# Kernel optimization log

Measured on AMD Instinct MI355X. Metric: run time of the kernel, lower is better.

The kernel has to match this reference:

```python
import jax, jax.numpy as jnp
import numpy as np

N_WORDS = 500000
N_LABELS = 64
PAD_INDEX = 0
UNK_INDEX = 1
BATCH, SEQ_LEN = 8192, 512


def setup_inputs() -> dict:
    key = jax.random.key(0)
    kw, kl, klen = jax.random.split(key, 3)
    # sequence lengths in [S/2, S]; pads go at the end (loop semantics assume contiguous prefix)
    lens = jax.random.randint(klen, (BATCH,), SEQ_LEN // 2, SEQ_LEN + 1)
    words = jax.random.randint(kw, (BATCH, SEQ_LEN), 2, N_WORDS, dtype=jnp.int32)
    labels = jax.random.randint(kl, (BATCH, SEQ_LEN), 0, N_LABELS, dtype=jnp.int32)
    pos = jnp.arange(SEQ_LEN, dtype=jnp.int32)[None, :]
    words = jnp.where(pos < lens[:, None], words, PAD_INDEX)
    trans_count = jnp.zeros((N_LABELS + 1, N_LABELS + 1), jnp.float32)
    emit_count = jnp.zeros((N_WORDS, N_LABELS), jnp.float32)
    return {"words": words, "labels": labels,
            "trans_count": trans_count, "emit_count": emit_count}


def reference(words, labels, trans_count, emit_count):
    # Vectorized equivalent of the double Python loop of scalar increments.
    B, S = words.shape
    lens = (words != PAD_INDEX).sum(-1)                       # [B]
    valid = jnp.arange(S, dtype=lens.dtype)[None, :] < lens[:, None]  # [B,S]
    wgt = valid.astype(trans_count.dtype).ravel()             # 1.0 for counted tokens
    ext_words = jnp.where(words >= N_WORDS, UNK_INDEX, words)
    # pre label: -1 (== last index N_LABELS) at j=0, else labels[:, j-1]
    pre = jnp.concatenate(
        [jnp.full((B, 1), N_LABELS, labels.dtype), labels[:, :-1]], axis=1)
    # trans_count[t, pre] += 1  (flattened scatter-add)
    t_flat = (labels.astype(jnp.int32) * (N_LABELS + 1) + pre.astype(jnp.int32)).ravel()
    tc = trans_count.ravel().at[t_flat].add(wgt).reshape(trans_count.shape)
    # emit_count[w, t] += 1
    e_flat = (ext_words.astype(jnp.int32) * N_LABELS + labels.astype(jnp.int32)).ravel()
    ec = emit_count.ravel().at[e_flat].add(wgt).reshape(emit_count.shape)
    return tc, ec
```

## Files before the change

### kernel.cpp

```cpp
#include <hip/hip_runtime.h>
#include <hip/hip_bf16.h>


constexpr int N_WORDS  = 500000;
constexpr int N_LABELS = 64;
constexpr int SEQ_LEN  = 512;
constexpr int BINS     = (N_LABELS + 1) * (N_LABELS + 1);
constexpr int N_CELLS  = N_WORDS * N_LABELS;
constexpr int P        = 1000;
constexpr int CPP      = 32000;
constexpr int TILE_TOK = 8192;
constexpr int QPT      = TILE_TOK / 4;
constexpr int B1 = 1024, G1 = 512;
constexpr int B2 = 1024;
constexpr int MAXTILES = 1024;
constexpr int FIN_BLOCKS = 5;
constexpr size_t DYN2 = (size_t)(CPP / 2 + MAXTILES) * sizeof(unsigned);


__global__ __launch_bounds__(B1)
void phase1(const int* __restrict__ words, const int* __restrict__ labels,
            unsigned* __restrict__ dir,
            unsigned short* __restrict__ keys,
            unsigned* __restrict__ part_t,
            int n, int ntiles) {
    __shared__ unsigned trans[BINS];
    __shared__ unsigned keybuf[TILE_TOK];
    __shared__ unsigned short sorted[TILE_TOK];
    __shared__ unsigned cnt[1024];
    __shared__ unsigned wsum[16];
    const int tid  = threadIdx.x;
    const int lane = tid & 63;
    for (int k = tid; k < BINS; k += B1) trans[k] = 0u;

    const int nquads = n >> 2;
    for (int tile = blockIdx.x; tile < ntiles; tile += gridDim.x) {
        const int q0 = tile * QPT;
        const int tq = min(QPT, nquads - q0);
        cnt[tid] = 0u;
        __syncthreads();

        for (int lq = tid; lq < tq; lq += B1) {
            const int q = q0 + lq;
            const int i = q << 2;
            const int4 w4 = reinterpret_cast<const int4*>(words)[q];
            const int4 l4 = reinterpret_cast<const int4*>(labels)[q];
            const int j0 = i & (SEQ_LEN - 1);
            int pre = (j0 == 0) ? N_LABELS : labels[i - 1];
            int wv[4] = {w4.x, w4.y, w4.z, w4.w};
            int lv[4] = {l4.x, l4.y, l4.z, l4.w};
            unsigned pk[4];
            #pragma unroll
            for (int k = 0; k < 4; ++k) {
                const int lab = lv[k];
                unsigned pack = 0xFFFFFFFFu;
                if (wv[k] != 0) {
                    atomicAdd(&trans[lab * (N_LABELS + 1) + pre], 1u);
                    const int w = (wv[k] >= N_WORDS) ? 1 : wv[k];
                    const unsigned key = (unsigned)w * N_LABELS + (unsigned)lab;
                    const unsigned p   = key / CPP;
                    pack = (p << 16) | (key - p * CPP);
                    atomicAdd(&cnt[p], 1u);
                }
                pk[k] = pack;
                pre = lab;
            }
            reinterpret_cast<uint4*>(keybuf)[lq] = make_uint4(pk[0], pk[1], pk[2], pk[3]);
        }
        __syncthreads();

        {
            const unsigned c = cnt[tid];
            unsigned v = c;
            #pragma unroll
            for (int d = 1; d < 64; d <<= 1) {
                const unsigned u = __shfl_up(v, d, 64);
                if (lane >= d) v += u;
            }
            if (lane == 63) wsum[tid >> 6] = v;
            __syncthreads();
            if (tid < 16) {
                const unsigned s = wsum[tid];
                unsigned vv = s;
                #pragma unroll
                for (int d = 1; d < 16; d <<= 1) {
                    const unsigned u = __shfl_up(vv, d, 64);
                    if (tid >= d) vv += u;
                }
                wsum[tid] = vv - s;
            }
            __syncthreads();
            const unsigned off = v - c + wsum[tid >> 6];
            cnt[tid] = off;
            if (tid < P) dir[(size_t)tile * P + tid] = (c << 16) | off;
        }
        __syncthreads();

        const int tt = tq << 2;
        for (int t = tid; t < tt; t += B1) {
            const unsigned pack = keybuf[t];
            if (pack != 0xFFFFFFFFu) {
                const unsigned s = atomicAdd(&cnt[pack >> 16], 1u);
                sorted[s] = (unsigned short)(pack & 0xFFFFu);
            }
        }
        __syncthreads();

        reinterpret_cast<uint4*>(keys + (size_t)tile * TILE_TOK)[tid] =
            reinterpret_cast<const uint4*>(sorted)[tid];
        __syncthreads();
    }

    unsigned* my = part_t + (size_t)blockIdx.x * BINS;
    for (int k = tid; k < BINS; k += B1) my[k] = trans[k];
}


__global__ __launch_bounds__(B2)
void phase2(const unsigned* __restrict__ dir,
            const unsigned short* __restrict__ keys,
            const unsigned* __restrict__ part_t,
            float* __restrict__ out, int ntiles) {
    extern __shared__ unsigned h[];
    unsigned* dcol = h + CPP / 2;
    const unsigned bid = blockIdx.x;

    if (bid < (unsigned)FIN_BLOCKS) {
        const int k = bid * B2 + threadIdx.x;
        if (k < BINS) {
            unsigned s = 0;
            #pragma unroll 8
            for (int pb = 0; pb < G1; ++pb) s += part_t[(size_t)pb * BINS + k];
            out[k] = (float)s;
        }
        return;
    }
    const unsigned p = bid - FIN_BLOCKS;

    for (int t = threadIdx.x; t < ntiles; t += B2)
        dcol[t] = dir[(size_t)t * P + p];

    for (int j = threadIdx.x; j < CPP / 8; j += B2)
        reinterpret_cast<uint4*>(h)[j] = make_uint4(0u, 0u, 0u, 0u);
    __syncthreads();

    const int nseg = ntiles << 1;
    for (int s = threadIdx.x; s < nseg; s += B2) {
        const int t = s >> 1, half = s & 1;
        const unsigned e = dcol[t];
        const unsigned c = e >> 16;
        const unsigned mid = (c + 1u) >> 1;
        const unsigned i0 = half ? mid : 0u;
        const unsigned i1 = half ? c : mid;
        const unsigned short* kp = keys + (size_t)t * TILE_TOK + (e & 0xFFFFu);
        for (unsigned i = i0; i < i1; ++i) {
            const unsigned loc = kp[i];
            atomicAdd(&h[loc >> 1], (loc & 1u) ? 65536u : 1u);
        }
    }
    __syncthreads();

    float* __restrict__ emit = out + BINS;
    float* dst = emit + (size_t)p * CPP;
    if (threadIdx.x < 3)
        dst[threadIdx.x] =
            (float)((h[threadIdx.x >> 1] >> ((threadIdx.x & 1u) * 16)) & 0xFFFFu);
    if (threadIdx.x == 3)
        dst[CPP - 1] = (float)(h[(CPP - 1) >> 1] >> 16);
    float4* dst4 = reinterpret_cast<float4*>(dst + 3);
    for (int u = threadIdx.x; u < (CPP - 4) / 4; u += B2) {
        const unsigned w0 = h[2 * u + 1];
        const unsigned w1 = h[2 * u + 2];
        const unsigned w2 = h[2 * u + 3];
        float4 f;
        f.x = (float)(w0 >> 16);
        f.y = (float)(w1 & 0xFFFFu);
        f.z = (float)(w1 >> 16);
        f.w = (float)(w2 & 0xFFFFu);
        dst4[u] = f;
    }
}


__global__ __launch_bounds__(256)
void zero_kernel(uint4* __restrict__ out, int out_quads, int out_size) {
    const uint4 z = {0u, 0u, 0u, 0u};
    const int stride = gridDim.x * blockDim.x;
    for (int q = blockIdx.x * blockDim.x + threadIdx.x; q < out_quads; q += stride)
        out[q] = z;
    if (blockIdx.x == 0 && threadIdx.x < (out_size & 3))
        ((unsigned*)out)[(out_quads << 2) + threadIdx.x] = 0u;
}

__global__ __launch_bounds__(1024)
void count_fallback(const int* __restrict__ words, const int* __restrict__ labels,
                    float* __restrict__ out, int nquads) {
    __shared__ unsigned hist[BINS];
    for (int k = threadIdx.x; k < BINS; k += 1024) hist[k] = 0u;
    __syncthreads();
    float* __restrict__ emit = out + BINS;
    const int stride = gridDim.x * blockDim.x;
    for (int q = blockIdx.x * blockDim.x + threadIdx.x; q < nquads; q += stride) {
        const int i = q << 2;
        const int4 w4 = reinterpret_cast<const int4*>(words)[q];
        const int4 l4 = reinterpret_cast<const int4*>(labels)[q];
        const int j0 = i & (SEQ_LEN - 1);
        int pre = (j0 == 0) ? N_LABELS : labels[i - 1];
        int wv[4] = {w4.x, w4.y, w4.z, w4.w};
        int lv[4] = {l4.x, l4.y, l4.z, l4.w};
        #pragma unroll
        for (int k = 0; k < 4; ++k) {
            const int w = wv[k], lab = lv[k];
            if (w != 0) {
                atomicAdd(&hist[lab * (N_LABELS + 1) + pre], 1u);
                const int we = (w >= N_WORDS) ? 1 : w;
                atomicAdd(&emit[(size_t)we * N_LABELS + lab], 1.0f);
            }
            pre = lab;
        }
    }
    __syncthreads();
    for (int k = threadIdx.x; k < BINS; k += 1024) {
        const unsigned c = hist[k];
        if (c) atomicAdd(&out[k], (float)c);
    }
}


extern "C" void kernel_launch(void* const* d_in, const int* in_sizes, int n_in,
                              void* d_out, int out_size, void* d_ws, size_t ws_size,
                              hipStream_t stream) {
    const int* words  = (const int*)d_in[0];
    const int* labels = (const int*)d_in[1];
    float* out = (float*)d_out;
    const int n = in_sizes[0];

    const int nquads = n >> 2;
    const int ntiles = (nquads + QPT - 1) / QPT;

    const size_t dir_bytes  = (size_t)ntiles * P * sizeof(unsigned);
    const size_t key_bytes  = (size_t)ntiles * TILE_TOK * sizeof(unsigned short);
    const size_t part_bytes = (size_t)G1 * BINS * sizeof(unsigned);
    const size_t dir_off  = 0;
    const size_t key_off  = dir_off + ((dir_bytes + 255) & ~size_t(255));
    const size_t part_off = key_off + ((key_bytes + 255) & ~size_t(255));
    const size_t need     = part_off + part_bytes;

    if (ws_size >= need && ntiles <= MAXTILES) {
        unsigned*       dir    = (unsigned*)((char*)d_ws + dir_off);
        unsigned short* keys   = (unsigned short*)((char*)d_ws + key_off);
        unsigned*       part_t = (unsigned*)((char*)d_ws + part_off);

        phase1<<<G1, B1, 0, stream>>>(words, labels, dir, keys, part_t, n, ntiles);
        phase2<<<P + FIN_BLOCKS, B2, DYN2, stream>>>(dir, keys, part_t, out, ntiles);
    } else {
        const int out_quads = out_size >> 2;
        zero_kernel<<<2048, 256, 0, stream>>>((uint4*)d_out, out_quads, out_size);
        count_fallback<<<512, 1024, 0, stream>>>(words, labels, out, nquads);
    }
}
```

Before: 254.3 us.

## Fuse sort and build phases into one cooperative kernel with grid sync

Merges the two-kernel pipeline (tile sort, then per-partition histogram build) into a single cooperative kernel. A grid-wide barrier separates the phases and shared memory is overlaid between them, with the grid sized from occupancy. This removes a kernel launch and the gap between launches. In exchange, the second phase now runs on at most one resident wave of blocks (likely 256 on MI355X) instead of 1005 independent blocks, which can hurt load balance. The sort loop also now reads packed keys as uint4.

```diff
diff --git a/kernel.cpp b/kernel.cpp
--- a/kernel.cpp
+++ b/kernel.cpp
@@ -1,5 +1,7 @@
 #include <hip/hip_runtime.h>
-#include <hip/hip_bf16.h>
+#include <hip/hip_cooperative_groups.h>
+
+namespace cg = cooperative_groups;
 
 
 constexpr int N_WORDS  = 500000;
@@ -11,141 +13,130 @@
 constexpr int CPP      = 32000;
 constexpr int TILE_TOK = 8192;
 constexpr int QPT      = TILE_TOK / 4;
-constexpr int B1 = 1024, G1 = 512;
-constexpr int B2 = 1024;
+constexpr int B        = 1024;
+constexpr int MAXG     = 512;
 constexpr int MAXTILES = 1024;
 constexpr int FIN_BLOCKS = 5;
-constexpr size_t DYN2 = (size_t)(CPP / 2 + MAXTILES) * sizeof(unsigned);
-
-
-__global__ __launch_bounds__(B1)
-void phase1(const int* __restrict__ words, const int* __restrict__ labels,
-            unsigned* __restrict__ dir,
-            unsigned short* __restrict__ keys,
-            unsigned* __restrict__ part_t,
-            int n, int ntiles) {
-    __shared__ unsigned trans[BINS];
-    __shared__ unsigned keybuf[TILE_TOK];
-    __shared__ unsigned short sorted[TILE_TOK];
-    __shared__ unsigned cnt[1024];
-    __shared__ unsigned wsum[16];
-    const int tid  = threadIdx.x;
-    const int lane = tid & 63;
-    for (int k = tid; k < BINS; k += B1) trans[k] = 0u;
-
-    const int nquads = n >> 2;
-    for (int tile = blockIdx.x; tile < ntiles; tile += gridDim.x) {
-        const int q0 = tile * QPT;
-        const int tq = min(QPT, nquads - q0);
-        cnt[tid] = 0u;
+
+constexpr int KEYBUF_OFF = 0;
+constexpr int TRANS_OFF  = 8192;
+constexpr int CNT_OFF    = TRANS_OFF + BINS;
+constexpr int WSUM_OFF   = CNT_OFF + 1024;
+constexpr int SORT_OFF   = WSUM_OFF + 16;
+constexpr int DYN_U32    = SORT_OFF + TILE_TOK/2;
+constexpr int DCOL_OFF   = CPP / 2;
+static_assert(DYN_U32 >= DCOL_OFF + MAXTILES, "overlay too small");
+constexpr size_t DYN_BYTES = (size_t)DYN_U32 * 4;
+
+
+__device__ __forceinline__ void tile_sort(const int* __restrict__ words,
+                                          const int* __restrict__ labels,
+                                          unsigned* __restrict__ dir,
+                                          unsigned short* __restrict__ keys,
+                                          unsigned* dyn, int tile, int nquads) {
+    const int tid = threadIdx.x, lane = tid & 63;
+    unsigned* keybuf = dyn + KEYBUF_OFF;
+    unsigned* trans  = dyn + TRANS_OFF;
+    unsigned* cnt    = dyn + CNT_OFF;
+    unsigned* wsum   = dyn + WSUM_OFF;
+    unsigned short* sorted = (unsigned short*)(dyn + SORT_OFF);
+
+    const int q0 = tile * QPT;
+    const int tq = min(QPT, nquads - q0);
+    cnt[tid] = 0u;
+    __syncthreads();
+
+    for (int lq = tid; lq < tq; lq += B) {
+        const int q = q0 + lq;
+        const int i = q << 2;
+        const int4 w4 = reinterpret_cast<const int4*>(words)[q];
+        const int4 l4 = reinterpret_cast<const int4*>(labels)[q];
+        const int j0 = i & (SEQ_LEN - 1);
+        int pre = (j0 == 0) ? N_LABELS : labels[i - 1];
+        int wv[4] = {w4.x, w4.y, w4.z, w4.w};
+        int lv[4] = {l4.x, l4.y, l4.z, l4.w};
+        unsigned pk[4];
+        #pragma unroll
+        for (int k = 0; k < 4; ++k) {
+            const int lab = lv[k];
+            unsigned pack = 0xFFFFFFFFu;
+            if (wv[k] != 0) {
+                atomicAdd(&trans[lab * (N_LABELS + 1) + pre], 1u);
+                const int w = (wv[k] >= N_WORDS) ? 1 : wv[k];
+                const unsigned key = (unsigned)w * N_LABELS + (unsigned)lab;
+                const unsigned p   = key / CPP;
+                pack = (p << 16) | (key - p * CPP);
+                atomicAdd(&cnt[p], 1u);
+            }
+            pk[k] = pack;
+            pre = lab;
+        }
+        reinterpret_cast<uint4*>(keybuf)[lq] = make_uint4(pk[0], pk[1], pk[2], pk[3]);
+    }
+    __syncthreads();
+
+    {
+        const unsigned c = cnt[tid];
+        unsigned v = c;
+        #pragma unroll
+        for (int d = 1; d < 64; d <<= 1) {
+            const unsigned u = __shfl_up(v, d, 64);
+            if (lane >= d) v += u;
+        }
+        if (lane == 63) wsum[tid >> 6] = v;
         __syncthreads();
-
-        for (int lq = tid; lq < tq; lq += B1) {
-            const int q = q0 + lq;
-            const int i = q << 2;
-            const int4 w4 = reinterpret_cast<const int4*>(words)[q];
-            const int4 l4 = reinterpret_cast<const int4*>(labels)[q];
-            const int j0 = i & (SEQ_LEN - 1);
-            int pre = (j0 == 0) ? N_LABELS : labels[i - 1];
-            int wv[4] = {w4.x, w4.y, w4.z, w4.w};
-            int lv[4] = {l4.x, l4.y, l4.z, l4.w};
-            unsigned pk[4];
+        if (tid < 16) {
+            const unsigned s = wsum[tid];
+            unsigned vv = s;
             #pragma unroll
-            for (int k = 0; k < 4; ++k) {
-                const int lab = lv[k];
-                unsigned pack = 0xFFFFFFFFu;
-                if (wv[k] != 0) {
-                    atomicAdd(&trans[lab * (N_LABELS + 1) + pre], 1u);
-                    const int w = (wv[k] >= N_WORDS) ? 1 : wv[k];
-                    const unsigned key = (unsigned)w * N_LABELS + (unsigned)lab;
-                    const unsigned p   = key / CPP;
-                    pack = (p << 16) | (key - p * CPP);
-                    atomicAdd(&cnt[p], 1u);
-                }
-                pk[k] = pack;
-                pre = lab;
-            }
-            reinterpret_cast<uint4*>(keybuf)[lq] = make_uint4(pk[0], pk[1], pk[2], pk[3]);
+            for (int d = 1; d < 16; d <<= 1) {
+                const unsigned u = __shfl_up(vv, d, 64);
+                if (tid >= d) vv += u;
+            }
+            wsum[tid] = vv - s;
         }
         __syncthreads();
-
-        {
-            const unsigned c = cnt[tid];
-            unsigned v = c;
-            #pragma unroll
-            for (int d = 1; d < 64; d <<= 1) {
-                const unsigned u = __shfl_up(v, d, 64);
-                if (lane >= d) v += u;
-            }
-            if (lane == 63) wsum[tid >> 6] = v;
-            __syncthreads();
-            if (tid < 16) {
-                const unsigned s = wsum[tid];
-                unsigned vv = s;
-                #pragma unroll
-                for (int d = 1; d < 16; d <<= 1) {
-                    const unsigned u = __shfl_up(vv, d, 64);
-                    if (tid >= d) vv += u;
-                }
-                wsum[tid] = vv - s;
-            }
-            __syncthreads();
-            const unsigned off = v - c + wsum[tid >> 6];
-            cnt[tid] = off;
-            if (tid < P) dir[(size_t)tile * P + tid] = (c << 16) | off;
-        }
-        __syncthreads();
-
-        const int tt = tq << 2;
-        for (int t = tid; t < tt; t += B1) {
-            const unsigned pack = keybuf[t];
+        const unsigned off = v - c + wsum[tid >> 6];
+        cnt[tid] = off;
+        if (tid < P) dir[(size_t)tile * P + tid] = (c << 16) | off;
+    }
+    __syncthreads();
+
+    for (int t4 = tid; t4 < tq; t4 += B) {
+        const uint4 pk4 = reinterpret_cast<const uint4*>(keybuf)[t4];
+        unsigned pks[4] = {pk4.x, pk4.y, pk4.z, pk4.w};
+        #pragma unroll
+        for (int k = 0; k < 4; ++k) {
+            const unsigned pack = pks[k];
             if (pack != 0xFFFFFFFFu) {
                 const unsigned s = atomicAdd(&cnt[pack >> 16], 1u);
                 sorted[s] = (unsigned short)(pack & 0xFFFFu);
             }
         }
-        __syncthreads();
-
-        reinterpret_cast<uint4*>(keys + (size_t)tile * TILE_TOK)[tid] =
-            reinterpret_cast<const uint4*>(sorted)[tid];
-        __syncthreads();
-    }
-
-    unsigned* my = part_t + (size_t)blockIdx.x * BINS;
-    for (int k = tid; k < BINS; k += B1) my[k] = trans[k];
-}
-
-
-__global__ __launch_bounds__(B2)
-void phase2(const unsigned* __restrict__ dir,
-            const unsigned short* __restrict__ keys,
-            const unsigned* __restrict__ part_t,
-            float* __restrict__ out, int ntiles) {
-    extern __shared__ unsigned h[];
-    unsigned* dcol = h + CPP / 2;
-    const unsigned bid = blockIdx.x;
-
-    if (bid < (unsigned)FIN_BLOCKS) {
-        const int k = bid * B2 + threadIdx.x;
-        if (k < BINS) {
-            unsigned s = 0;
-            #pragma unroll 8
-            for (int pb = 0; pb < G1; ++pb) s += part_t[(size_t)pb * BINS + k];
-            out[k] = (float)s;
-        }
-        return;
-    }
-    const unsigned p = bid - FIN_BLOCKS;
-
-    for (int t = threadIdx.x; t < ntiles; t += B2)
+    }
+    __syncthreads();
+
+    reinterpret_cast<uint4*>(keys + (size_t)tile * TILE_TOK)[tid] =
+        reinterpret_cast<const uint4*>(sorted)[tid];
+    __syncthreads();
+}
+
+__device__ __forceinline__ void part_build(const unsigned* __restrict__ dir,
+                                           const unsigned short* __restrict__ keys,
+                                           float* __restrict__ out,
+                                           unsigned* dyn, int p, int ntiles) {
+    unsigned* h    = dyn;
+    unsigned* dcol = dyn + DCOL_OFF;
+    const int tid = threadIdx.x;
+
+    for (int t = tid; t < ntiles; t += B)
         dcol[t] = dir[(size_t)t * P + p];
-
-    for (int j = threadIdx.x; j < CPP / 8; j += B2)
+    for (int j = tid; j < CPP / 8; j += B)
         reinterpret_cast<uint4*>(h)[j] = make_uint4(0u, 0u, 0u, 0u);
     __syncthreads();
 
     const int nseg = ntiles << 1;
-    for (int s = threadIdx.x; s < nseg; s += B2) {
+    for (int s = tid; s < nseg; s += B) {
         const int t = s >> 1, half = s & 1;
         const unsigned e = dcol[t];
         const unsigned c = e >> 16;
@@ -162,13 +153,12 @@
 
     float* __restrict__ emit = out + BINS;
     float* dst = emit + (size_t)p * CPP;
-    if (threadIdx.x < 3)
-        dst[threadIdx.x] =
-            (float)((h[threadIdx.x >> 1] >> ((threadIdx.x & 1u) * 16)) & 0xFFFFu);
-    if (threadIdx.x == 3)
+    if (tid < 3)
+        dst[tid] = (float)((h[tid >> 1] >> ((tid & 1u) * 16)) & 0xFFFFu);
+    if (tid == 3)
         dst[CPP - 1] = (float)(h[(CPP - 1) >> 1] >> 16);
     float4* dst4 = reinterpret_cast<float4*>(dst + 3);
-    for (int u = threadIdx.x; u < (CPP - 4) / 4; u += B2) {
+    for (int u = tid; u < (CPP - 4) / 4; u += B) {
         const unsigned w0 = h[2 * u + 1];
         const unsigned w1 = h[2 * u + 2];
         const unsigned w2 = h[2 * u + 3];
@@ -179,6 +169,80 @@
         f.w = (float)(w2 & 0xFFFFu);
         dst4[u] = f;
     }
+}
+
+
+__global__ __launch_bounds__(B)
+void fused(const int* __restrict__ words, const int* __restrict__ labels,
+           unsigned* __restrict__ dir, unsigned short* __restrict__ keys,
+           unsigned* __restrict__ part_t, float* __restrict__ out,
+           int n, int ntiles) {
+    extern __shared__ unsigned dyn[];
+    cg::grid_group grid = cg::this_grid();
+    const int tid = threadIdx.x, bid = blockIdx.x, G = gridDim.x;
+
+    unsigned* trans = dyn + TRANS_OFF;
+    for (int k = tid; k < BINS; k += B) trans[k] = 0u;
+
+    const int nquads = n >> 2;
+    for (int tile = bid; tile < ntiles; tile += G)
+        tile_sort(words, labels, dir, keys, dyn, tile, nquads);
+
+    {
+        unsigned* my = part_t + (size_t)bid * BINS;
+        for (int k = tid; k < BINS; k += B) my[k] = trans[k];
+    }
+    grid.sync();
+
+    const int W = P + FIN_BLOCKS;
+    for (int w = bid; w < W; w += G) {
+        __syncthreads();
+        if (w < FIN_BLOCKS) {
+            const int k = w * B + tid;
+            if (k < BINS) {
+                unsigned s = 0;
+                for (int pb = 0; pb < G; ++pb) s += part_t[(size_t)pb * BINS + k];
+                out[k] = (float)s;
+            }
+            continue;
+        }
+        part_build(dir, keys, out, dyn, w - FIN_BLOCKS, ntiles);
+    }
+}
+
+
+__global__ __launch_bounds__(B)
+void phase1_k(const int* __restrict__ words, const int* __restrict__ labels,
+              unsigned* __restrict__ dir, unsigned short* __restrict__ keys,
+              unsigned* __restrict__ part_t, int n, int ntiles) {
+    extern __shared__ unsigned dyn[];
+    const int tid = threadIdx.x;
+    unsigned* trans = dyn + TRANS_OFF;
+    for (int k = tid; k < BINS; k += B) trans[k] = 0u;
+    const int nquads = n >> 2;
+    for (int tile = blockIdx.x; tile < ntiles; tile += gridDim.x)
+        tile_sort(words, labels, dir, keys, dyn, tile, nquads);
+    unsigned* my = part_t + (size_t)blockIdx.x * BINS;
+    for (int k = tid; k < BINS; k += B) my[k] = trans[k];
+}
+
+__global__ __launch_bounds__(B)
+void phase2_k(const unsigned* __restrict__ dir,
+              const unsigned short* __restrict__ keys,
+              const unsigned* __restrict__ part_t,
+              float* __restrict__ out, int ntiles, int g1) {
+    extern __shared__ unsigned dyn[];
+    const unsigned bid = blockIdx.x;
+    if (bid < (unsigned)FIN_BLOCKS) {
+        const int k = bid * B + threadIdx.x;
+        if (k < BINS) {
+            unsigned s = 0;
+            for (int pb = 0; pb < g1; ++pb) s += part_t[(size_t)pb * BINS + k];
+            out[k] = (float)s;
+        }
+        return;
+    }
+    part_build(dir, keys, out, dyn, bid - FIN_BLOCKS, ntiles);
 }
 
 
@@ -240,19 +304,44 @@
 
     const size_t dir_bytes  = (size_t)ntiles * P * sizeof(unsigned);
     const size_t key_bytes  = (size_t)ntiles * TILE_TOK * sizeof(unsigned short);
-    const size_t part_bytes = (size_t)G1 * BINS * sizeof(unsigned);
+    const size_t part_bytes = (size_t)MAXG * BINS * sizeof(unsigned);
     const size_t dir_off  = 0;
     const size_t key_off  = dir_off + ((dir_bytes + 255) & ~size_t(255));
     const size_t part_off = key_off + ((key_bytes + 255) & ~size_t(255));
     const size_t need     = part_off + part_bytes;
 
+    static int G = 0;
+    if (G == 0) {
+        int nb = 0;
+        if (hipOccupancyMaxActiveBlocksPerMultiprocessor(
+                &nb, (const void*)fused, B, DYN_BYTES) != hipSuccess || nb < 1)
+            nb = 1;
+        int dev = 0; hipGetDevice(&dev);
+        hipDeviceProp_t prop;
+        int cus = (hipGetDeviceProperties(&prop, dev) == hipSuccess)
+                      ? prop.multiProcessorCount : 256;
+        int g = nb * cus;
+        G = g < 1 ? 1 : (g > MAXG ? MAXG : g);
+    }
+
     if (ws_size >= need && ntiles <= MAXTILES) {
         unsigned*       dir    = (unsigned*)((char*)d_ws + dir_off);
         unsigned short* keys   = (unsigned short*)((char*)d_ws + key_off);
         unsigned*       part_t = (unsigned*)((char*)d_ws + part_off);
 
-        phase1<<<G1, B1, 0, stream>>>(words, labels, dir, keys, part_t, n, ntiles);
-        phase2<<<P + FIN_BLOCKS, B2, DYN2, stream>>>(dir, keys, part_t, out, ntiles);
+        void* args[] = {(void*)&words, (void*)&labels, (void*)&dir,
+                        (void*)&keys, (void*)&part_t, (void*)&out,
+                        (void*)&n, (void*)&ntiles};
+        const bool ok = (hipLaunchCooperativeKernel(
+            (const void*)fused, dim3(G), dim3(B), args, DYN_BYTES, stream)
+            == hipSuccess);
+        if (!ok) {
+            const int g1 = MAXG;
+            phase1_k<<<g1, B, DYN_BYTES, stream>>>(words, labels, dir, keys,
+                                                   part_t, n, ntiles);
+            phase2_k<<<P + FIN_BLOCKS, B, DYN_BYTES, stream>>>(dir, keys, part_t,
+                                                               out, ntiles, g1);
+        }
     } else {
         const int out_quads = out_size >> 2;
         zero_kernel<<<2048, 256, 0, stream>>>((uint4*)d_out, out_quads, out_size);
```

Result: slower. 322.9 us (+27.0%).
